# Kernel tuning notes

Hardware: AMD Instinct MI355X
Metric: run time of the kernel (lower is better)

Reference implementation:

```python
import jax, jax.numpy as jnp
import numpy as np

T = 2048        # num tokens
HID = 2048      # hidden_size
HQ = 16         # num_heads
HKV = 8         # num_kv_heads
D = 128         # head_dim
P = 2           # power retention exponent
THETA = 10000.0 # rope base
SCALE = D ** -0.5


def setup_inputs() -> dict:
    key = jax.random.key(0)
    ks = jax.random.split(key, 8)
    s = 0.02
    return {
        "positions": jnp.arange(T, dtype=jnp.int64) if jax.config.jax_enable_x64 else jnp.arange(T, dtype=jnp.int32),
        "hidden_states": jax.random.normal(ks[0], (T, HID), jnp.float32),
        "Wq": jax.random.normal(ks[1], (HID, HQ * D), jnp.float32) * s,
        "bq": jnp.zeros((HQ * D,), jnp.float32),
        "Wk": jax.random.normal(ks[2], (HID, HKV * D), jnp.float32) * s,
        "bk": jnp.zeros((HKV * D,), jnp.float32),
        "Wv": jax.random.normal(ks[3], (HID, HKV * D), jnp.float32) * s,
        "bv": jnp.zeros((HKV * D,), jnp.float32),
        "Wg": jax.random.normal(ks[4], (HID, HKV), jnp.float32) * s,
        "bg": jnp.zeros((HKV,), jnp.float32),
        "Wo": jax.random.normal(ks[5], (HQ * D, HID), jnp.float32) * s,
        "bo": jnp.zeros((HID,), jnp.float32),
    }


def _rope_neox(x, pos):
    # x: [T, H, D], pos: [T]; rotate-half (neox) style, rotary_dim == head_dim
    half = D // 2
    inv_freq = 1.0 / (THETA ** (jnp.arange(0, D, 2, dtype=jnp.float32) / D))  # [D/2]
    freqs = pos.astype(jnp.float32)[:, None] * inv_freq                        # [T, D/2]
    cos = jnp.cos(freqs)[:, None, :]
    sin = jnp.sin(freqs)[:, None, :]
    x1, x2 = x[..., :half], x[..., half:]
    return jnp.concatenate([x1 * cos - x2 * sin, x2 * cos + x1 * sin], axis=-1)


def reference(positions, hidden_states, Wq, bq, Wk, bk, Wv, bv, Wg, bg, Wo, bo):
    # QKVG projections
    q = (hidden_states @ Wq + bq).reshape(T, HQ, D)
    k = (hidden_states @ Wk + bk).reshape(T, HKV, D)
    v = (hidden_states @ Wv + bv).reshape(T, HKV, D)
    g = hidden_states @ Wg + bg            # [T, HKV], one gate scalar per kv head

    # RoPE on q/k, logsigmoid gate in fp32
    q = _rope_neox(q, positions)
    k = _rope_neox(k, positions)
    g = jax.nn.log_sigmoid(g.astype(jnp.float32))   # [T, HKV], <= 0
    G = jnp.cumsum(g, axis=0)                       # [T, HKV] cumulative log-decay

    # GQA: expand kv heads to query heads
    rep = HQ // HKV
    k = jnp.repeat(k, rep, axis=1)   # [T, HQ, D]
    v = jnp.repeat(v, rep, axis=1)
    G = jnp.repeat(G, rep, axis=1)   # [T, HQ]

    # Power retention (quadratic attention form, seq_len <= switch_over_seq_len):
    # W_ij = (scale * q_i . k_j)^p * exp(G_i - G_j), causal j <= i
    S = jnp.einsum('thd,shd->hts', q, k) * SCALE      # [H, T, T]
    S = S ** P
    Gh = G.T                                          # [H, T]
    mask = jnp.tril(jnp.ones((T, T), dtype=bool))
    diff = jnp.where(mask[None], Gh[:, :, None] - Gh[:, None, :], -jnp.inf)
    W = S * jnp.exp(diff)                             # decay<=1 inside mask, 0 outside

    out = jnp.einsum('hts,shd->thd', W, v)            # [T, H, D]
    out = out.reshape(T, HQ * D) @ Wo + bo            # o_proj
    return out
```

## Files before the change

kernel.cpp:

```cpp
#include <hip/hip_runtime.h>
#include <hip/hip_bf16.h>
#include <math.h>

#define T_SEQ 2048
#define HID 2048
#define HQ 16
#define HKV 8
#define D_HEAD 128
#define HALF 64
#define SCALE_F 0.08838834764831845f
#define PROJW 4096

typedef __attribute__((ext_vector_type(8))) short bf16x8;
typedef __attribute__((ext_vector_type(4))) float f32x4;

static __device__ __forceinline__ short f2bf(float x) {
  unsigned u = __builtin_bit_cast(unsigned, x);
  unsigned r = (u + 0x7FFF + ((u >> 16) & 1)) >> 16;
  return (short)r;
}
static __device__ __forceinline__ float bf2f(unsigned short u) {
  unsigned v = ((unsigned)u) << 16;
  return __builtin_bit_cast(float, v);
}

#define GLDS(gsrc, ldst) \
  __builtin_amdgcn_global_load_lds((const __attribute__((address_space(1))) void*)(gsrc), \
                                   (__attribute__((address_space(3))) void*)(ldst), 16, 0, 0)

__global__ __launch_bounds__(256)
void transpose_all(const float* __restrict__ Wq, const float* __restrict__ Wk,
                   const float* __restrict__ Wv, const float* __restrict__ Wo,
                   short* __restrict__ BTall, short* __restrict__ WoT)
{
  const int bx = blockIdx.x;
  const int k0 = blockIdx.y * 32;
  const float* src; short* dst; int Nsrc, n0;
  if (bx < 64)       { src = Wq; Nsrc = 2048; dst = BTall;                       n0 = bx * 32; }
  else if (bx < 96)  { src = Wk; Nsrc = 1024; dst = BTall + (size_t)2048 * 2048; n0 = (bx - 64) * 32; }
  else if (bx < 128) { src = Wv; Nsrc = 1024; dst = BTall + (size_t)3072 * 2048; n0 = (bx - 96) * 32; }
  else               { src = Wo; Nsrc = 2048; dst = WoT;                         n0 = (bx - 128) * 32; }

  __shared__ float tile[32][33];
  const int r = threadIdx.x >> 5, c = threadIdx.x & 31;
  #pragma unroll
  for (int i = 0; i < 4; ++i)
    tile[r + i * 8][c] = src[(size_t)(k0 + r + i * 8) * Nsrc + n0 + c];
  __syncthreads();
  const int n = threadIdx.x >> 3, k4 = (threadIdx.x & 7) * 4;
  short4 o;
  o.x = f2bf(tile[k4 + 0][n]); o.y = f2bf(tile[k4 + 1][n]);
  o.z = f2bf(tile[k4 + 2][n]); o.w = f2bf(tile[k4 + 3][n]);
  *reinterpret_cast<short4*>(&dst[(size_t)(n0 + n) * 2048 + k0 + k4]) = o;
}

__global__ __launch_bounds__(256)
void add_f32(float* __restrict__ out, const float* __restrict__ part, int n4)
{
  int i = blockIdx.x * blockDim.x + threadIdx.x;
  if (i >= n4) return;
  float4 a = reinterpret_cast<float4*>(out)[i];
  const float4 b = reinterpret_cast<const float4*>(part)[i];
  a.x += b.x; a.y += b.y; a.z += b.z; a.w += b.w;
  reinterpret_cast<float4*>(out)[i] = a;
}

template <bool OBF>
__global__ __launch_bounds__(256)
void gemm3b(const short* __restrict__ A, const short* __restrict__ BT,
            const float* __restrict__ b0, const float* __restrict__ b1,
            const float* __restrict__ b2, int s1, int s2,
            void* __restrict__ Cout0, void* __restrict__ Cout1,
            int N, int Kst, int klen)
{
  __shared__ short As[3][128 * 32];
  __shared__ short Bs[3][128 * 32];
  const int tid = threadIdx.x;
  const int wave = tid >> 6, lane = tid & 63;
  const int bm0 = blockIdx.y * 128, bn0 = blockIdx.x * 128;
  const int z = blockIdx.z;
  const int koff = z * klen;
  const int wm = (wave >> 1) * 64, wn = (wave & 1) * 64;

  const int srow = wave * 32 + (lane >> 2);
  const int scol = (lane & 3) * 8;
  const short* Abase = A + (size_t)(bm0 + srow) * Kst + koff + scol;
  const short* Bbase = BT + (size_t)(bn0 + srow) * Kst + koff + scol;

  f32x4 acc[4][4] = {};
  const int nk = klen >> 5;

#define STAGE(buf, kk)                                                           \
  do {                                                                           \
    GLDS(Abase + ((kk) << 5), &As[buf][(wave * 32) * 32]);                       \
    GLDS(Abase + ((kk) << 5) + (size_t)16 * Kst, &As[buf][(wave * 32 + 16) * 32]); \
    GLDS(Bbase + ((kk) << 5), &Bs[buf][(wave * 32) * 32]);                       \
    GLDS(Bbase + ((kk) << 5) + (size_t)16 * Kst, &Bs[buf][(wave * 32 + 16) * 32]); \
  } while (0)

  STAGE(0, 0);
  if (nk > 1) {
    STAGE(1, 1);
    asm volatile("s_waitcnt vmcnt(4)" ::: "memory");
  } else {
    asm volatile("s_waitcnt vmcnt(0)" ::: "memory");
  }
  __builtin_amdgcn_s_barrier();
  __builtin_amdgcn_sched_barrier(0);

  const int kof = (lane >> 4) * 8;
  const int rA = wm + (lane & 15);
  const int rB = wn + (lane & 15);

  for (int t = 0; t < nk; ++t) {
    const int p = t % 3, sb = (t + 2) % 3;
    if (t + 2 < nk) STAGE(sb, t + 2);

    bf16x8 af[4], bfr[4];
    #pragma unroll
    for (int i = 0; i < 4; ++i) {
      af[i]  = *reinterpret_cast<const bf16x8*>(&As[p][(rA + i * 16) * 32 + kof]);
      bfr[i] = *reinterpret_cast<const bf16x8*>(&Bs[p][(rB + i * 16) * 32 + kof]);
    }
    #pragma unroll
    for (int i = 0; i < 4; ++i)
      #pragma unroll
      for (int j = 0; j < 4; ++j)
        acc[i][j] = __builtin_amdgcn_mfma_f32_16x16x32_bf16(af[i], bfr[j], acc[i][j], 0, 0, 0);

    if (t + 1 < nk) {
      __builtin_amdgcn_sched_barrier(0);
      if (t + 2 < nk) asm volatile("s_waitcnt vmcnt(4)" ::: "memory");
      else            asm volatile("s_waitcnt vmcnt(0)" ::: "memory");
      __builtin_amdgcn_s_barrier();
      __builtin_amdgcn_sched_barrier(0);
    }
  }

  void* Cout = z ? Cout1 : Cout0;
  const int crow = wm + (lane >> 4) * 4;
  const int ccol = wn + (lane & 15);
  #pragma unroll
  for (int j = 0; j < 4; ++j) {
    const int col = bn0 + ccol + j * 16;
    float b = 0.f;
    if (z == 0)
      b = (col < s1) ? b0[col] : ((col < s2) ? b1[col - s1] : b2[col - s2]);
    #pragma unroll
    for (int i = 0; i < 4; ++i)
      #pragma unroll
      for (int r = 0; r < 4; ++r) {
        const int row = bm0 + crow + i * 16 + r;
        const float v = acc[i][j][r] + b;
        if constexpr (OBF)
          ((short*)Cout)[(size_t)row * N + col] = f2bf(v);
        else
          ((float*)Cout)[(size_t)row * N + col] = v;
      }
  }
#undef STAGE
}

__global__ __launch_bounds__(256)
void gproj_kernel(const float* __restrict__ hs, const float* __restrict__ Wg,
                  const float* __restrict__ bg, float* __restrict__ gT,
                  short* __restrict__ hsb)
{
  const int t = blockIdx.x, tid = threadIdx.x;
  __shared__ float red[256][9];
  float a[8] = {0.f, 0.f, 0.f, 0.f, 0.f, 0.f, 0.f, 0.f};
  for (int cc = tid; cc < HID; cc += 256) {
    const float hv = hs[(size_t)t * HID + cc];
    hsb[(size_t)t * HID + cc] = f2bf(hv);
    const float4 w0 = *reinterpret_cast<const float4*>(Wg + (size_t)cc * 8);
    const float4 w1 = *reinterpret_cast<const float4*>(Wg + (size_t)cc * 8 + 4);
    a[0] = fmaf(hv, w0.x, a[0]); a[1] = fmaf(hv, w0.y, a[1]);
    a[2] = fmaf(hv, w0.z, a[2]); a[3] = fmaf(hv, w0.w, a[3]);
    a[4] = fmaf(hv, w1.x, a[4]); a[5] = fmaf(hv, w1.y, a[5]);
    a[6] = fmaf(hv, w1.z, a[6]); a[7] = fmaf(hv, w1.w, a[7]);
  }
  #pragma unroll
  for (int j = 0; j < 8; ++j) red[tid][j] = a[j];
  __syncthreads();
  for (int s = 128; s >= 1; s >>= 1) {
    if (tid < s) {
      #pragma unroll
      for (int j = 0; j < 8; ++j) red[tid][j] += red[tid + s][j];
    }
    __syncthreads();
  }
  if (tid < 8) {
    const float x = red[0][tid] + bg[tid];
    const float nx = -x;
    const float sp = (nx > 20.f) ? nx : log1pf(expf(nx));
    gT[(size_t)tid * T_SEQ + t] = -sp;
  }
}

__global__ __launch_bounds__(512)
void gscan_kernel(const float* __restrict__ gT, float* __restrict__ Gct)
{
  const int h = blockIdx.x;
  const int tid = threadIdx.x;
  const int wid = tid >> 6, lane = tid & 63;
  __shared__ float wsum[8];

  const float4 v = reinterpret_cast<const float4*>(gT + (size_t)h * T_SEQ)[tid];
  const float p0 = v.x, p1 = p0 + v.y, p2 = p1 + v.z, p3 = p2 + v.w;

  float sc = p3;
  #pragma unroll
  for (int off = 1; off < 64; off <<= 1) {
    const float o = __shfl_up(sc, off, 64);
    if (lane >= off) sc += o;
  }
  if (lane == 63) wsum[wid] = sc;
  __syncthreads();
  float wof = 0.f;
  #pragma unroll
  for (int w = 0; w < 8; ++w) wof += (w < wid) ? wsum[w] : 0.f;

  const float excl = wof + sc - p3;
  reinterpret_cast<float4*>(Gct + (size_t)h * T_SEQ)[tid] =
      make_float4(excl + p0, excl + p1, excl + p2, excl + p3);
}

__global__ __launch_bounds__(256)
void rope_vtrans(short* __restrict__ proj, unsigned short* __restrict__ vt)
{
  __shared__ float cs[64], sn[64];
  __shared__ unsigned short tile[32][33];

  if (blockIdx.x < 2048) {
    const int t = blockIdx.x;
    if (threadIdx.x < 64) {
      const int i = threadIdx.x;
      const float f = (float)t * powf(10000.0f, -(float)i / 64.0f);
      cs[i] = cosf(f); sn[i] = sinf(f);
    }
    __syncthreads();
    const int u = threadIdx.x;
    if (u < 192) {
      const int hh = u >> 3, ch = u & 7;
      short* base = proj + (size_t)t * PROJW +
                    ((hh < HQ) ? hh * D_HEAD : 2048 + (hh - HQ) * D_HEAD);
      bf16x8 x1 = *reinterpret_cast<bf16x8*>(base + ch * 8);
      bf16x8 x2 = *reinterpret_cast<bf16x8*>(base + HALF + ch * 8);
      #pragma unroll
      for (int j = 0; j < 8; ++j) {
        const float a = bf2f((unsigned short)x1[j]);
        const float b = bf2f((unsigned short)x2[j]);
        const float cc = cs[ch * 8 + j], ss = sn[ch * 8 + j];
        x1[j] = f2bf(a * cc - b * ss);
        x2[j] = f2bf(b * cc + a * ss);
      }
      *reinterpret_cast<bf16x8*>(base + ch * 8) = x1;
      *reinterpret_cast<bf16x8*>(base + HALF + ch * 8) = x2;
    }
  } else {
    const int idx = blockIdx.x - 2048;
    const int tt = (idx & 63) * 32, dd = ((idx >> 6) & 3) * 32, hk = idx >> 8;
    const unsigned short* pj = (const unsigned short*)proj;
    const int c = threadIdx.x & 31, r0 = (threadIdx.x >> 5) * 4;
    #pragma unroll
    for (int i = 0; i < 4; ++i)
      tile[r0 + i][c] = pj[(size_t)(tt + r0 + i) * PROJW + 3072 + hk * 128 + dd + c];
    __syncthreads();
    #pragma unroll
    for (int i = 0; i < 4; ++i)
      vt[(size_t)(hk * 128 + dd + r0 + i) * T_SEQ + tt + c] = tile[c][r0 + i];
  }
}

__global__ __launch_bounds__(256, 1)
void attn_mfma(const short* __restrict__ proj, const short* __restrict__ vt,
               const float* __restrict__ Gct, short* __restrict__ outb)
{
  __shared__ __align__(16) char smem[86528];
  const int hk = blockIdx.x;
  const int tb = blockIdx.y * 64;
  const int tid = threadIdx.x;
  const int wid = tid >> 6, lane = tid & 63;
  const int c = lane & 15, g = lane >> 4;
  const int h = 2 * hk + (wid >> 1);
  const int tw = tb + (wid & 1) * 32;
  const float* Gh = Gct + (size_t)hk * T_SEQ;

  const float glim = Gh[tb] + 90.0f;
  int lo = 0, hi = tb;
  while (lo < hi) {
    const int mid = (lo + hi) >> 1;
    if (Gh[mid] > glim) lo = mid + 1; else hi = mid;
  }
  const int sfirst = lo & ~63;
  const int nst = ((tb - sfirst) >> 6) + 1;

  bf16x8 qf[2][4];
  #pragma unroll
  for (int tt = 0; tt < 2; ++tt)
    #pragma unroll
    for (int kb = 0; kb < 4; ++kb)
      qf[tt][kb] = *reinterpret_cast<const bf16x8*>(
          proj + (size_t)(tw + 16 * tt + c) * PROJW + h * D_HEAD + kb * 32 + g * 8);
  const float gt0 = Gh[tw + c];
  const float gt1 = Gh[tw + 16 + c];
  const float gtw = Gh[tw];
  const int twmax = tw + 31;

  f32x4 accv[2][8] = {};

#define ASTG(buf, s64)                                                                   \
  do {                                                                                   \
    _Pragma("unroll")                                                                    \
    for (int i2 = 0; i2 < 4; ++i2) {                                                     \
      const int cid = tid + 256 * i2;                                                    \
      const int kr = cid >> 4, kc = cid & 15;                                            \
      GLDS(proj + (size_t)((s64) + kr) * PROJW + 2048 + hk * 128 + ((kc ^ (kr & 7)) * 8),\
           smem + (buf) * 16384 + cid * 16);                                             \
      const int vr = cid >> 3, vc = cid & 7;                                             \
      GLDS(vt + (size_t)(hk * 128 + vr) * T_SEQ + (s64) + ((vc ^ (vr & 7)) * 8),         \
           smem + 32768 + (buf) * 16384 + cid * 16);                                     \
    }                                                                                    \
    if (tid < 64) ((float*)(smem + 86016))[(buf) * 64 + tid] = Gh[(s64) + tid];          \
  } while (0)

  ASTG(0, sfirst);
  __syncthreads();

  for (int i = 0; i < nst; ++i) {
    const int cur = i & 1;
    if (i + 1 < nst) ASTG(cur ^ 1, sfirst + (i + 1) * 64);
    const int sbase64 = sfirst + i * 64;
    const float* Gss = (const float*)(smem + 86016) + cur * 64;
    char* Pmy = smem + 65536 + wid * 5120;

    #pragma unroll
    for (int st = 0; st < 2; ++st) {
      const int s0 = sbase64 + st * 32;
      if (s0 > twmax) continue;
      if (gtw - Gss[st * 32 + 31] < -90.0f) continue;

      bf16x8 kf[2][4];
      #pragma unroll
      for (int sg = 0; sg < 2; ++sg)
        #pragma unroll
        for (int kb = 0; kb < 4; ++kb) {
          const int row = st * 32 + 16 * sg + c;
          const int byt = (row * 256 + kb * 64 + g * 16) ^ ((c & 7) << 4);
          kf[sg][kb] = *reinterpret_cast<const bf16x8*>(smem + cur * 16384 + byt);
        }
      f32x4 sa[2][2] = {};
      #pragma unroll
      for (int kb = 0; kb < 4; ++kb)
        #pragma unroll
        for (int sg = 0; sg < 2; ++sg)
          #pragma unroll
          for (int tt = 0; tt < 2; ++tt)
            sa[sg][tt] = __builtin_amdgcn_mfma_f32_16x16x32_bf16(
                kf[sg][kb], qf[tt][kb], sa[sg][tt], 0, 0, 0);

      #pragma unroll
      for (int sg = 0; sg < 2; ++sg) {
        const float4 gs = *reinterpret_cast<const float4*>(&Gss[st * 32 + sg * 16 + g * 4]);
        const float gsv[4] = {gs.x, gs.y, gs.z, gs.w};
        #pragma unroll
        for (int tt = 0; tt < 2; ++tt) {
          const int tg = tw + 16 * tt + c;
          const float gt = tt ? gt1 : gt0;
          const int sg0 = s0 + sg * 16 + g * 4;
          float w[4];
          #pragma unroll
          for (int r = 0; r < 4; ++r) {
            const float dv = sa[sg][tt][r] * SCALE_F;
            const float ww = dv * dv * __expf(gt - gsv[r]);
            w[r] = (sg0 + r <= tg) ? ww : 0.0f;
          }
          uint2 pv;
          pv.x = ((unsigned)(unsigned short)f2bf(w[1]) << 16) | (unsigned short)f2bf(w[0]);
          pv.y = ((unsigned)(unsigned short)f2bf(w[3]) << 16) | (unsigned short)f2bf(w[2]);
          *reinterpret_cast<uint2*>(Pmy + st * 2560 + (c + 16 * tt) * 80 + 8 * g + 32 * sg) = pv;
        }
      }
      asm volatile("s_waitcnt lgkmcnt(0)" ::: "memory");
      __builtin_amdgcn_sched_barrier(0);

      bf16x8 pf[2];
      #pragma unroll
      for (int tt = 0; tt < 2; ++tt)
        pf[tt] = *reinterpret_cast<const bf16x8*>(Pmy + st * 2560 + (c + 16 * tt) * 80 + g * 16);

      #pragma unroll
      for (int db = 0; db < 8; ++db) {
        const int row = 16 * db + c;
        const int byt = (row * 128 + st * 64 + g * 16) ^ ((c & 7) << 4);
        const bf16x8 vf = *reinterpret_cast<const bf16x8*>(smem + 32768 + cur * 16384 + byt);
        #pragma unroll
        for (int tt = 0; tt < 2; ++tt)
          accv[tt][db] = __builtin_amdgcn_mfma_f32_16x16x32_bf16(pf[tt], vf, accv[tt][db], 0, 0, 0);
      }
    }
    __syncthreads();
  }

  char* Wme = smem + wid * 8704;
  #pragma unroll
  for (int tt = 0; tt < 2; ++tt)
    #pragma unroll
    for (int db = 0; db < 8; ++db)
      #pragma unroll
      for (int r = 0; r < 4; ++r)
        *reinterpret_cast<short*>(Wme + (16 * tt + 4 * g + r) * 272 + (16 * db + c) * 2)
            = f2bf(accv[tt][db][r]);
  asm volatile("s_waitcnt lgkmcnt(0)" ::: "memory");
  __builtin_amdgcn_sched_barrier(0);
  #pragma unroll
  for (int e = 0; e < 8; ++e) {
    const int idx = e * 64 + lane;
    const int tr = idx >> 4, d0 = (idx & 15) * 8;
    const bf16x8 vv = *reinterpret_cast<const bf16x8*>(Wme + tr * 272 + d0 * 2);
    *reinterpret_cast<bf16x8*>(outb + ((size_t)(tw + tr) * HQ + h) * D_HEAD + d0) = vv;
  }
#undef ASTG
}

extern "C" void kernel_launch(void* const* d_in, const int* in_sizes, int n_in,
                              void* d_out, int out_size, void* d_ws, size_t ws_size,
                              hipStream_t stream)
{
  const float* hs = (const float*)d_in[1];
  const float* Wq = (const float*)d_in[2];
  const float* bq = (const float*)d_in[3];
  const float* Wk = (const float*)d_in[4];
  const float* bk = (const float*)d_in[5];
  const float* Wv = (const float*)d_in[6];
  const float* bv = (const float*)d_in[7];
  const float* Wg = (const float*)d_in[8];
  const float* bg = (const float*)d_in[9];
  const float* Wo = (const float*)d_in[10];
  const float* bo = (const float*)d_in[11];
  float* outp = (float*)d_out;

  short* proj  = (short*)d_ws;
  short* vtb   = proj + (size_t)T_SEQ * PROJW;
  float* gT    = (float*)(vtb + (size_t)HKV * D_HEAD * T_SEQ);
  float* Gct   = gT + 16384;
  short* hsb   = (short*)(Gct + 16384);
  short* BTall = hsb + (size_t)2048 * 2048;
  short* WoT   = BTall + (size_t)4096 * 2048;
  short* attnout = hsb;
  float* opart   = (float*)BTall;

  transpose_all<<<dim3(192, 64), 256, 0, stream>>>(Wq, Wk, Wv, Wo, BTall, WoT);

  gproj_kernel<<<2048, 256, 0, stream>>>(hs, Wg, bg, gT, hsb);
  gscan_kernel<<<8, 512, 0, stream>>>(gT, Gct);

  gemm3b<true><<<dim3(32, 16, 1), 256, 0, stream>>>(
      hsb, BTall, bq, bk, bv, 2048, 3072, proj, proj, PROJW, 2048, 2048);

  rope_vtrans<<<4096, 256, 0, stream>>>(proj, (unsigned short*)vtb);

  attn_mfma<<<dim3(8, 32), 256, 0, stream>>>(proj, vtb, Gct, attnout);

  gemm3b<false><<<dim3(16, 16, 2), 256, 0, stream>>>(
      attnout, WoT, bo, bo, bo, 1 << 30, 1 << 30, outp, opart, 2048, 2048, 1024);
  add_f32<<<4096, 256, 0, stream>>>(outp, opart, 1048576);
}
```

Baseline: 140.2 us.

## Use 64x128 GEMM tiles and drop split-K with separate add pass

Replaces the 128x128 tiled GEMM with a 64x128 tile variant (two M-fragments per wave) and raises occupancy via launch bounds. The o_proj GEMM no longer uses split-K with a second partial buffer and a follow-up add kernel; it instead launches twice as many M-tiles over full K. MFMA issue is wrapped in setprio to favour math waves. The aim is more blocks to fill the CUs and one fewer kernel launch plus partial-sum traffic, at the cost of lower per-block data reuse.

```diff
diff --git a/kernel.cpp b/kernel.cpp
--- a/kernel.cpp
+++ b/kernel.cpp
@@ -54,104 +54,93 @@
   *reinterpret_cast<short4*>(&dst[(size_t)(n0 + n) * 2048 + k0 + k4]) = o;
 }
 
-__global__ __launch_bounds__(256)
-void add_f32(float* __restrict__ out, const float* __restrict__ part, int n4)
-{
-  int i = blockIdx.x * blockDim.x + threadIdx.x;
-  if (i >= n4) return;
-  float4 a = reinterpret_cast<float4*>(out)[i];
-  const float4 b = reinterpret_cast<const float4*>(part)[i];
-  a.x += b.x; a.y += b.y; a.z += b.z; a.w += b.w;
-  reinterpret_cast<float4*>(out)[i] = a;
-}
-
 template <bool OBF>
-__global__ __launch_bounds__(256)
-void gemm3b(const short* __restrict__ A, const short* __restrict__ BT,
+__global__ __launch_bounds__(256, 4)
+void gemm64(const short* __restrict__ A, const short* __restrict__ BT,
             const float* __restrict__ b0, const float* __restrict__ b1,
             const float* __restrict__ b2, int s1, int s2,
-            void* __restrict__ Cout0, void* __restrict__ Cout1,
-            int N, int Kst, int klen)
-{
-  __shared__ short As[3][128 * 32];
-  __shared__ short Bs[3][128 * 32];
-  const int tid = threadIdx.x;
-  const int wave = tid >> 6, lane = tid & 63;
-  const int bm0 = blockIdx.y * 128, bn0 = blockIdx.x * 128;
-  const int z = blockIdx.z;
-  const int koff = z * klen;
-  const int wm = (wave >> 1) * 64, wn = (wave & 1) * 64;
-
-  const int srow = wave * 32 + (lane >> 2);
-  const int scol = (lane & 3) * 8;
-  const short* Abase = A + (size_t)(bm0 + srow) * Kst + koff + scol;
-  const short* Bbase = BT + (size_t)(bn0 + srow) * Kst + koff + scol;
-
-  f32x4 acc[4][4] = {};
-  const int nk = klen >> 5;
-
-#define STAGE(buf, kk)                                                           \
-  do {                                                                           \
-    GLDS(Abase + ((kk) << 5), &As[buf][(wave * 32) * 32]);                       \
-    GLDS(Abase + ((kk) << 5) + (size_t)16 * Kst, &As[buf][(wave * 32 + 16) * 32]); \
-    GLDS(Bbase + ((kk) << 5), &Bs[buf][(wave * 32) * 32]);                       \
-    GLDS(Bbase + ((kk) << 5) + (size_t)16 * Kst, &Bs[buf][(wave * 32 + 16) * 32]); \
+            void* __restrict__ Cout, int N, int K)
+{
+  __shared__ short Al[3][64 * 32];
+  __shared__ short Bl[3][128 * 32];
+  const int tid = threadIdx.x, wid = tid >> 6, lane = tid & 63;
+  const int bm0 = blockIdx.y * 64, bn0 = blockIdx.x * 128;
+  const int wr = wid >> 1, wc = wid & 1;
+  const int c = lane & 15, g = lane >> 4;
+  const int lrow = lane >> 2, lcol = (lane & 3) * 8;
+  const int nk = K >> 5;
+
+  f32x4 acc[2][4] = {};
+
+#define STAGE(buf, kt)                                                          \
+  do {                                                                          \
+    _Pragma("unroll")                                                           \
+    for (int e = 0; e < 3; ++e) {                                               \
+      const int ch = wid * 3 + e;                                               \
+      if (ch < 4)                                                               \
+        GLDS(A + (size_t)(bm0 + ch * 16 + lrow) * K + (kt) * 32 + lcol,         \
+             (char*)&Al[buf][0] + ch * 1024);                                   \
+      else                                                                      \
+        GLDS(BT + (size_t)(bn0 + (ch - 4) * 16 + lrow) * K + (kt) * 32 + lcol,  \
+             (char*)&Bl[buf][0] + (ch - 4) * 1024);                             \
+    }                                                                           \
   } while (0)
 
   STAGE(0, 0);
   if (nk > 1) {
     STAGE(1, 1);
-    asm volatile("s_waitcnt vmcnt(4)" ::: "memory");
+    asm volatile("s_waitcnt vmcnt(3)" ::: "memory");
   } else {
     asm volatile("s_waitcnt vmcnt(0)" ::: "memory");
   }
   __builtin_amdgcn_s_barrier();
   __builtin_amdgcn_sched_barrier(0);
-
-  const int kof = (lane >> 4) * 8;
-  const int rA = wm + (lane & 15);
-  const int rB = wn + (lane & 15);
 
   for (int t = 0; t < nk; ++t) {
     const int p = t % 3, sb = (t + 2) % 3;
     if (t + 2 < nk) STAGE(sb, t + 2);
 
-    bf16x8 af[4], bfr[4];
-    #pragma unroll
-    for (int i = 0; i < 4; ++i) {
-      af[i]  = *reinterpret_cast<const bf16x8*>(&As[p][(rA + i * 16) * 32 + kof]);
-      bfr[i] = *reinterpret_cast<const bf16x8*>(&Bs[p][(rB + i * 16) * 32 + kof]);
-    }
-    #pragma unroll
-    for (int i = 0; i < 4; ++i)
-      #pragma unroll
-      for (int j = 0; j < 4; ++j)
-        acc[i][j] = __builtin_amdgcn_mfma_f32_16x16x32_bf16(af[i], bfr[j], acc[i][j], 0, 0, 0);
+    bf16x8 aR[2], bR[4];
+    #pragma unroll
+    for (int mf = 0; mf < 2; ++mf)
+      aR[mf] = *reinterpret_cast<const bf16x8*>(
+          (char*)&Al[p][0] + (wr * 32 + mf * 16 + c) * 64 + g * 16);
+    #pragma unroll
+    for (int nf = 0; nf < 4; ++nf)
+      bR[nf] = *reinterpret_cast<const bf16x8*>(
+          (char*)&Bl[p][0] + (wc * 64 + nf * 16 + c) * 64 + g * 16);
+    asm volatile("s_waitcnt lgkmcnt(0)" ::: "memory");
+    __builtin_amdgcn_sched_barrier(0);
+
+    __builtin_amdgcn_s_setprio(1);
+    #pragma unroll
+    for (int mf = 0; mf < 2; ++mf)
+      #pragma unroll
+      for (int nf = 0; nf < 4; ++nf)
+        acc[mf][nf] = __builtin_amdgcn_mfma_f32_16x16x32_bf16(aR[mf], bR[nf], acc[mf][nf], 0, 0, 0);
+    __builtin_amdgcn_s_setprio(0);
 
     if (t + 1 < nk) {
       __builtin_amdgcn_sched_barrier(0);
-      if (t + 2 < nk) asm volatile("s_waitcnt vmcnt(4)" ::: "memory");
+      if (t + 2 < nk) asm volatile("s_waitcnt vmcnt(3)" ::: "memory");
       else            asm volatile("s_waitcnt vmcnt(0)" ::: "memory");
       __builtin_amdgcn_s_barrier();
       __builtin_amdgcn_sched_barrier(0);
     }
   }
 
-  void* Cout = z ? Cout1 : Cout0;
-  const int crow = wm + (lane >> 4) * 4;
-  const int ccol = wn + (lane & 15);
-  #pragma unroll
-  for (int j = 0; j < 4; ++j) {
-    const int col = bn0 + ccol + j * 16;
-    float b = 0.f;
-    if (z == 0)
-      b = (col < s1) ? b0[col] : ((col < s2) ? b1[col - s1] : b2[col - s2]);
-    #pragma unroll
-    for (int i = 0; i < 4; ++i)
+  const int crow = bm0 + wr * 32 + g * 4;
+  const int ccol = bn0 + wc * 64 + c;
+  #pragma unroll
+  for (int nf = 0; nf < 4; ++nf) {
+    const int col = ccol + nf * 16;
+    const float b = (col < s1) ? b0[col] : ((col < s2) ? b1[col - s1] : b2[col - s2]);
+    #pragma unroll
+    for (int mf = 0; mf < 2; ++mf)
       #pragma unroll
       for (int r = 0; r < 4; ++r) {
-        const int row = bm0 + crow + i * 16 + r;
-        const float v = acc[i][j][r] + b;
+        const int row = crow + mf * 16 + r;
+        const float v = acc[mf][nf][r] + b;
         if constexpr (OBF)
           ((short*)Cout)[(size_t)row * N + col] = f2bf(v);
         else
@@ -448,21 +437,19 @@
   short* BTall = hsb + (size_t)2048 * 2048;
   short* WoT   = BTall + (size_t)4096 * 2048;
   short* attnout = hsb;
-  float* opart   = (float*)BTall;
 
   transpose_all<<<dim3(192, 64), 256, 0, stream>>>(Wq, Wk, Wv, Wo, BTall, WoT);
 
   gproj_kernel<<<2048, 256, 0, stream>>>(hs, Wg, bg, gT, hsb);
   gscan_kernel<<<8, 512, 0, stream>>>(gT, Gct);
 
-  gemm3b<true><<<dim3(32, 16, 1), 256, 0, stream>>>(
-      hsb, BTall, bq, bk, bv, 2048, 3072, proj, proj, PROJW, 2048, 2048);
+  gemm64<true><<<dim3(32, 32), 256, 0, stream>>>(
+      hsb, BTall, bq, bk, bv, 2048, 3072, proj, PROJW, 2048);
 
   rope_vtrans<<<4096, 256, 0, stream>>>(proj, (unsigned short*)vtb);
 
   attn_mfma<<<dim3(8, 32), 256, 0, stream>>>(proj, vtb, Gct, attnout);
 
-  gemm3b<false><<<dim3(16, 16, 2), 256, 0, stream>>>(
-      attnout, WoT, bo, bo, bo, 1 << 30, 1 << 30, outp, opart, 2048, 2048, 1024);
-  add_f32<<<4096, 256, 0, stream>>>(outp, opart, 1048576);
-}
+  gemm64<false><<<dim3(16, 32), 256, 0, stream>>>(
+      attnout, WoT, bo, bo, bo, 1 << 30, 1 << 30, outp, 2048, 2048);
+}
```

After: 151.2 us. 1.08x slower.

## Replace projection GEMM with 256x128x64 swizzled-LDS tile kernel and workgroup remap

Applied to the files above, without the earlier changes.

Replaces the 128x128x32 GEMM with a larger 256x128 tile and K-step of 64, held in triple-buffered LDS with an XOR swizzle to avoid bank conflicts. It also remaps workgroup IDs for better cache locality, splits each K-step into two halves of fragment reads overlapped with MFMAs, and raises wave priority around the MFMA blocks. Each block now does more reuse per loaded byte. The cost is much larger LDS use (about 144KB) and more registers, which forces one block per CU, and fewer blocks in the grid, which may leave some CUs idle.

```diff
diff --git a/kernel.cpp b/kernel.cpp
--- a/kernel.cpp
+++ b/kernel.cpp
@@ -66,71 +66,108 @@
 }
 
 template <bool OBF>
-__global__ __launch_bounds__(256)
-void gemm3b(const short* __restrict__ A, const short* __restrict__ BT,
-            const float* __restrict__ b0, const float* __restrict__ b1,
-            const float* __restrict__ b2, int s1, int s2,
-            void* __restrict__ Cout0, void* __restrict__ Cout1,
-            int N, int Kst, int klen)
-{
-  __shared__ short As[3][128 * 32];
-  __shared__ short Bs[3][128 * 32];
-  const int tid = threadIdx.x;
-  const int wave = tid >> 6, lane = tid & 63;
-  const int bm0 = blockIdx.y * 128, bn0 = blockIdx.x * 128;
+__global__ __launch_bounds__(256, 1)
+void gemmF(const short* __restrict__ A, const short* __restrict__ BT,
+           const float* __restrict__ b0, const float* __restrict__ b1,
+           const float* __restrict__ b2, int s1, int s2,
+           void* __restrict__ Cout0, void* __restrict__ Cout1,
+           int N, int Kst, int klen)
+{
+  __shared__ short Al[3][256 * 64];
+  __shared__ short Bl[3][128 * 64];
+  const int tid = threadIdx.x, wid = tid >> 6, lane = tid & 63;
   const int z = blockIdx.z;
   const int koff = z * klen;
-  const int wm = (wave >> 1) * 64, wn = (wave & 1) * 64;
-
-  const int srow = wave * 32 + (lane >> 2);
-  const int scol = (lane & 3) * 8;
-  const short* Abase = A + (size_t)(bm0 + srow) * Kst + koff + scol;
-  const short* Bbase = BT + (size_t)(bn0 + srow) * Kst + koff + scol;
-
-  f32x4 acc[4][4] = {};
-  const int nk = klen >> 5;
-
-#define STAGE(buf, kk)                                                           \
-  do {                                                                           \
-    GLDS(Abase + ((kk) << 5), &As[buf][(wave * 32) * 32]);                       \
-    GLDS(Abase + ((kk) << 5) + (size_t)16 * Kst, &As[buf][(wave * 32 + 16) * 32]); \
-    GLDS(Bbase + ((kk) << 5), &Bs[buf][(wave * 32) * 32]);                       \
-    GLDS(Bbase + ((kk) << 5) + (size_t)16 * Kst, &Bs[buf][(wave * 32 + 16) * 32]); \
+  const int nwg = gridDim.x * gridDim.y;
+  const int orig = blockIdx.y * gridDim.x + blockIdx.x;
+  const int swz = (orig & 7) * (nwg >> 3) + (orig >> 3);
+  const int bx = swz % gridDim.x, by = swz / gridDim.x;
+  const int bm0 = by * 256, bn0 = bx * 128;
+  const int wr = wid >> 1, wc = wid & 1;
+  const int c = lane & 15, g = lane >> 4;
+  const int xc = (c & 7) << 4;
+  const int nk = klen >> 6;
+
+  f32x4 acc[8][4] = {};
+
+#define STGA(p, kt, j) do {                                                   \
+    const int cid = (j) * 256 + tid;                                          \
+    const int rr = cid >> 3;                                                  \
+    const int gx = (cid & 7) ^ (rr & 7);                                      \
+    GLDS(A + (size_t)(bm0 + rr) * Kst + koff + (kt) * 64 + gx * 8,            \
+         (char*)&Al[p][0] + ((j) * 256 + wid * 64) * 16);                     \
   } while (0)
+#define STGB(p, kt, j) do {                                                   \
+    const int cid = (j) * 256 + tid;                                          \
+    const int rr = cid >> 3;                                                  \
+    const int gx = (cid & 7) ^ (rr & 7);                                      \
+    GLDS(BT + (size_t)(bn0 + rr) * Kst + koff + (kt) * 64 + gx * 8,           \
+         (char*)&Bl[p][0] + ((j) * 256 + wid * 64) * 16);                     \
+  } while (0)
+#define STAGE(p, kt) do {                                                     \
+    STGA(p, kt, 0); STGA(p, kt, 1); STGA(p, kt, 2); STGA(p, kt, 3);           \
+    STGA(p, kt, 4); STGA(p, kt, 5); STGA(p, kt, 6); STGA(p, kt, 7);           \
+    STGB(p, kt, 0); STGB(p, kt, 1); STGB(p, kt, 2); STGB(p, kt, 3);           \
+  } while (0)
+
+#define RDA(p, mf, ks)                                                        \
+  (*reinterpret_cast<const bf16x8*>((const char*)&Al[p][0] +                  \
+      (size_t)(wr * 128 + (mf) * 16 + c) * 128 + (((ks) * 64 + g * 16) ^ xc)))
+#define RDB(p, nf, ks)                                                        \
+  (*reinterpret_cast<const bf16x8*>((const char*)&Bl[p][0] +                  \
+      (size_t)(wc * 64 + (nf) * 16 + c) * 128 + (((ks) * 64 + g * 16) ^ xc)))
 
   STAGE(0, 0);
   if (nk > 1) {
     STAGE(1, 1);
-    asm volatile("s_waitcnt vmcnt(4)" ::: "memory");
+    asm volatile("s_waitcnt vmcnt(12)" ::: "memory");
   } else {
     asm volatile("s_waitcnt vmcnt(0)" ::: "memory");
   }
   __builtin_amdgcn_s_barrier();
   __builtin_amdgcn_sched_barrier(0);
-
-  const int kof = (lane >> 4) * 8;
-  const int rA = wm + (lane & 15);
-  const int rB = wn + (lane & 15);
 
   for (int t = 0; t < nk; ++t) {
     const int p = t % 3, sb = (t + 2) % 3;
     if (t + 2 < nk) STAGE(sb, t + 2);
 
-    bf16x8 af[4], bfr[4];
-    #pragma unroll
-    for (int i = 0; i < 4; ++i) {
-      af[i]  = *reinterpret_cast<const bf16x8*>(&As[p][(rA + i * 16) * 32 + kof]);
-      bfr[i] = *reinterpret_cast<const bf16x8*>(&Bs[p][(rB + i * 16) * 32 + kof]);
-    }
-    #pragma unroll
-    for (int i = 0; i < 4; ++i)
-      #pragma unroll
-      for (int j = 0; j < 4; ++j)
-        acc[i][j] = __builtin_amdgcn_mfma_f32_16x16x32_bf16(af[i], bfr[j], acc[i][j], 0, 0, 0);
+    bf16x8 a0[8], br0[4];
+    #pragma unroll
+    for (int mf = 0; mf < 8; ++mf) a0[mf] = RDA(p, mf, 0);
+    #pragma unroll
+    for (int nf = 0; nf < 4; ++nf) br0[nf] = RDB(p, nf, 0);
+    asm volatile("s_waitcnt lgkmcnt(0)" ::: "memory");
+    __builtin_amdgcn_sched_barrier(0);
+
+    bf16x8 a1[8], br1[4];
+    #pragma unroll
+    for (int mf = 0; mf < 8; ++mf) a1[mf] = RDA(p, mf, 1);
+    #pragma unroll
+    for (int nf = 0; nf < 4; ++nf) br1[nf] = RDB(p, nf, 1);
+    __builtin_amdgcn_sched_barrier(0);
+
+    __builtin_amdgcn_s_setprio(1);
+    #pragma unroll
+    for (int mf = 0; mf < 8; ++mf)
+      #pragma unroll
+      for (int nf = 0; nf < 4; ++nf)
+        acc[mf][nf] = __builtin_amdgcn_mfma_f32_16x16x32_bf16(a0[mf], br0[nf], acc[mf][nf], 0, 0, 0);
+    __builtin_amdgcn_s_setprio(0);
+
+    asm volatile("s_waitcnt lgkmcnt(0)" ::: "memory");
+    __builtin_amdgcn_sched_barrier(0);
+
+    __builtin_amdgcn_s_setprio(1);
+    #pragma unroll
+    for (int mf = 0; mf < 8; ++mf)
+      #pragma unroll
+      for (int nf = 0; nf < 4; ++nf)
+        acc[mf][nf] = __builtin_amdgcn_mfma_f32_16x16x32_bf16(a1[mf], br1[nf], acc[mf][nf], 0, 0, 0);
+    __builtin_amdgcn_s_setprio(0);
 
     if (t + 1 < nk) {
       __builtin_amdgcn_sched_barrier(0);
-      if (t + 2 < nk) asm volatile("s_waitcnt vmcnt(4)" ::: "memory");
+      if (t + 2 < nk) asm volatile("s_waitcnt vmcnt(12)" ::: "memory");
       else            asm volatile("s_waitcnt vmcnt(0)" ::: "memory");
       __builtin_amdgcn_s_barrier();
       __builtin_amdgcn_sched_barrier(0);
@@ -138,27 +175,31 @@
   }
 
   void* Cout = z ? Cout1 : Cout0;
-  const int crow = wm + (lane >> 4) * 4;
-  const int ccol = wn + (lane & 15);
-  #pragma unroll
-  for (int j = 0; j < 4; ++j) {
-    const int col = bn0 + ccol + j * 16;
+  const int crow = bm0 + wr * 128 + g * 4;
+  const int ccol = bn0 + wc * 64 + c;
+  #pragma unroll
+  for (int nf = 0; nf < 4; ++nf) {
+    const int col = ccol + nf * 16;
     float b = 0.f;
     if (z == 0)
       b = (col < s1) ? b0[col] : ((col < s2) ? b1[col - s1] : b2[col - s2]);
     #pragma unroll
-    for (int i = 0; i < 4; ++i)
+    for (int mf = 0; mf < 8; ++mf)
       #pragma unroll
       for (int r = 0; r < 4; ++r) {
-        const int row = bm0 + crow + i * 16 + r;
-        const float v = acc[i][j][r] + b;
+        const int row = crow + mf * 16 + r;
+        const float v = acc[mf][nf][r] + b;
         if constexpr (OBF)
           ((short*)Cout)[(size_t)row * N + col] = f2bf(v);
         else
           ((float*)Cout)[(size_t)row * N + col] = v;
       }
   }
+#undef STGA
+#undef STGB
 #undef STAGE
+#undef RDA
+#undef RDB
 }
 
 __global__ __launch_bounds__(256)
@@ -455,14 +496,14 @@
   gproj_kernel<<<2048, 256, 0, stream>>>(hs, Wg, bg, gT, hsb);
   gscan_kernel<<<8, 512, 0, stream>>>(gT, Gct);
 
-  gemm3b<true><<<dim3(32, 16, 1), 256, 0, stream>>>(
+  gemmF<true><<<dim3(32, 8, 1), 256, 0, stream>>>(
       hsb, BTall, bq, bk, bv, 2048, 3072, proj, proj, PROJW, 2048, 2048);
 
   rope_vtrans<<<4096, 256, 0, stream>>>(proj, (unsigned short*)vtb);
 
   attn_mfma<<<dim3(8, 32), 256, 0, stream>>>(proj, vtb, Gct, attnout);
 
-  gemm3b<false><<<dim3(16, 16, 2), 256, 0, stream>>>(
+  gemmF<false><<<dim3(16, 8, 2), 256, 0, stream>>>(
       attnout, WoT, bo, bo, bo, 1 << 30, 1 << 30, outp, opart, 2048, 2048, 1024);
   add_f32<<<4096, 256, 0, stream>>>(outp, opart, 1048576);
 }
```

Measured after the change: 152.5 us. +8.8%, slower.
